# Performance work log

Measured on AMD Instinct MI355X. Metric: run time of the kernel, lower is better.

The kernel has to match this reference:

```python
import jax, jax.numpy as jnp
import numpy as np

NUM_SUBGRAPH = 4096  # static number of segments (subgraph_idx.max() + 1)


def setup_inputs() -> dict:
    key = jax.random.key(0)
    k1, k2, k3, k4 = jax.random.split(key, 4)
    E, K = 4194304, 20
    label = jax.random.randint(k1, (E,), 0, 2).astype(jnp.float32)      # 0/1 edge labels
    log_theta = jax.random.normal(k2, (E, K), dtype=jnp.float32)        # Bernoulli logits per mixture comp
    log_alpha = jax.random.normal(k3, (E, K), dtype=jnp.float32)        # mixture logits per edge
    subgraph_idx = jax.random.randint(k4, (E,), 0, NUM_SUBGRAPH)        # segment id per edge
    return {"label": label, "log_theta": log_theta, "log_alpha": log_alpha,
            "subgraph_idx": subgraph_idx}


def reference(label, log_theta, log_alpha, subgraph_idx):
    E, K = log_theta.shape
    S = NUM_SUBGRAPH
    # BCEWithLogits(reduction='none'), vectorized over all K components:
    # softplus(x) - x*y  ==  -(y*log sigmoid(x) + (1-y)*log(1-sigmoid(x)))
    adj_loss = jax.nn.softplus(log_theta) - log_theta * label[:, None]  # [E, K]
    # segment reductions keyed by subgraph_idx
    const = jax.ops.segment_sum(jnp.ones((E,), log_theta.dtype), subgraph_idx,
                                num_segments=S)                          # [S]
    reduce_adj_loss = jax.ops.segment_sum(adj_loss, subgraph_idx,
                                          num_segments=S)                # [S, K]
    reduce_log_alpha = jax.ops.segment_sum(log_alpha, subgraph_idx,
                                           num_segments=S)               # [S, K]
    reduce_log_alpha = reduce_log_alpha / const[:, None]
    reduce_log_alpha = jax.nn.log_softmax(reduce_log_alpha, axis=-1)
    log_prob = jax.scipy.special.logsumexp(-reduce_adj_loss + reduce_log_alpha, axis=1)  # [S]
    loss = -jnp.sum(log_prob) / jnp.asarray(E, log_theta.dtype)
    return loss
```

## Files before the change

kernel.cpp:

```cpp
#include <hip/hip_runtime.h>
#include <stdint.h>


#define S_SEG 4096
#define K_COMP 20

__device__ __forceinline__ float sp_f(float x) {
    return fmaxf(x, 0.f) + __logf(1.f + __expf(-fabsf(x)));
}

__device__ __forceinline__ void gatomic_add_f(float* p, float v) {
    __hip_atomic_fetch_add(p, v, __ATOMIC_RELAXED, __HIP_MEMORY_SCOPE_AGENT);
}

__global__ __launch_bounds__(256) void pack_count_kernel(
    const int* __restrict__ sidx, const float* __restrict__ label,
    unsigned short* __restrict__ packed, unsigned int* __restrict__ g_cnt,
    int E4, int doPack)
{
    __shared__ unsigned int hist[S_SEG];
    for (int i = threadIdx.x; i < S_SEG; i += 256) hist[i] = 0u;
    __syncthreads();

    const int4*   s4 = (const int4*)sidx;
    const float4* l4 = (const float4*)label;
    int gt = blockIdx.x * 256 + threadIdx.x;
    int stride = gridDim.x * 256;
    for (int i = gt; i < E4; i += stride) {
        int4   sv = s4[i];
        float4 lv = l4[i];
        atomicAdd(&hist[sv.x & 4095], 1u);
        atomicAdd(&hist[sv.y & 4095], 1u);
        atomicAdd(&hist[sv.z & 4095], 1u);
        atomicAdd(&hist[sv.w & 4095], 1u);
        if (doPack) {
            ushort4 pk;
            pk.x = (unsigned short)((sv.x & 4095) | (lv.x != 0.f ? 0x8000 : 0));
            pk.y = (unsigned short)((sv.y & 4095) | (lv.y != 0.f ? 0x8000 : 0));
            pk.z = (unsigned short)((sv.z & 4095) | (lv.z != 0.f ? 0x8000 : 0));
            pk.w = (unsigned short)((sv.w & 4095) | (lv.w != 0.f ? 0x8000 : 0));
            ((ushort4*)packed)[i] = pk;
        }
    }
    __syncthreads();
    for (int i = threadIdx.x; i < S_SEG; i += 256) {
        unsigned int c = hist[i];
        if (c) atomicAdd(&g_cnt[i], c);
    }
}

template<bool PACKED>
__global__ __launch_bounds__(256) void seg_accum_kernel(
    const float* __restrict__ theta, const float* __restrict__ alpha,
    const unsigned short* __restrict__ packed,
    const int* __restrict__ sidx, const float* __restrict__ label,
    float* __restrict__ g_adj, float* __restrict__ g_alp,
    int ntiles)
{
    __shared__ float tab[4 * S_SEG];
    for (int i = threadIdx.x; i < 4 * S_SEG; i += 256) tab[i] = 0.f;
    __syncthreads();

    const int  role  = blockIdx.x;
    const bool isAdj = role < 5;
    const int  c4    = isAdj ? role : role - 5;
    const float4* src4 = (const float4*)(isAdj ? theta : alpha);
    const int nY = gridDim.y;

    for (int t = blockIdx.y; t < ntiles; t += 2 * nY) {
        const int tB = t + nY;
        const bool hasB = (tB < ntiles);

        int eA = t * 256 + threadIdx.x;
        float4 vA = src4[(size_t)eA * 5 + c4];
        int sA; float labA;
        if (PACKED) {
            unsigned short p = packed[eA];
            sA = p & 4095; labA = (p & 0x8000) ? 1.f : 0.f;
        } else {
            sA = sidx[eA] & 4095; labA = label[eA];
        }

        int eB = 0; float4 vB; int sB = 0; float labB = 0.f;
        if (hasB) {
            eB = tB * 256 + threadIdx.x;
            vB = src4[(size_t)eB * 5 + c4];
            if (PACKED) {
                unsigned short p = packed[eB];
                sB = p & 4095; labB = (p & 0x8000) ? 1.f : 0.f;
            } else {
                sB = sidx[eB] & 4095; labB = label[eB];
            }
        }

        if (isAdj) {
            vA.x = sp_f(vA.x) - vA.x * labA;
            vA.y = sp_f(vA.y) - vA.y * labA;
            vA.z = sp_f(vA.z) - vA.z * labA;
            vA.w = sp_f(vA.w) - vA.w * labA;
        }
        atomicAdd(&tab[            sA], vA.x);
        atomicAdd(&tab[1 * S_SEG + sA], vA.y);
        atomicAdd(&tab[2 * S_SEG + sA], vA.z);
        atomicAdd(&tab[3 * S_SEG + sA], vA.w);

        if (hasB) {
            if (isAdj) {
                vB.x = sp_f(vB.x) - vB.x * labB;
                vB.y = sp_f(vB.y) - vB.y * labB;
                vB.z = sp_f(vB.z) - vB.z * labB;
                vB.w = sp_f(vB.w) - vB.w * labB;
            }
            atomicAdd(&tab[            sB], vB.x);
            atomicAdd(&tab[1 * S_SEG + sB], vB.y);
            atomicAdd(&tab[2 * S_SEG + sB], vB.z);
            atomicAdd(&tab[3 * S_SEG + sB], vB.w);
        }
    }
    __syncthreads();

    float* g = isAdj ? g_adj : g_alp;
    const int k0 = c4 * 4;
    for (int j = threadIdx.x; j < 4 * S_SEG; j += 256) {
        int kk = j >> 12;
        int s  = j & 4095;
        gatomic_add_f(&g[s * K_COMP + k0 + kk], tab[j]);
    }
}

__global__ __launch_bounds__(256) void finalize_kernel(
    const float* __restrict__ g_adj, const float* __restrict__ g_alp,
    const unsigned int* __restrict__ g_cnt, float* __restrict__ out, float Ef)
{
    float local = 0.f;
    for (int s = threadIdx.x; s < S_SEG; s += 256) {
        float c = (float)g_cnt[s];
        if (c < 1.f) c = 1.f;
        float inv = 1.f / c;

        float a[K_COMP];
        float am = -1e30f;
        #pragma unroll
        for (int k = 0; k < K_COMP; ++k) {
            a[k] = g_alp[s * K_COMP + k] * inv;
            am = fmaxf(am, a[k]);
        }
        float den = 0.f;
        #pragma unroll
        for (int k = 0; k < K_COMP; ++k) den += __expf(a[k] - am);
        float lse = am + __logf(den);

        float t[K_COMP];
        float tm = -1e30f;
        #pragma unroll
        for (int k = 0; k < K_COMP; ++k) {
            t[k] = (a[k] - lse) - g_adj[s * K_COMP + k];
            tm = fmaxf(tm, t[k]);
        }
        float d2 = 0.f;
        #pragma unroll
        for (int k = 0; k < K_COMP; ++k) d2 += __expf(t[k] - tm);
        local += tm + __logf(d2);
    }

    __shared__ float red[256];
    red[threadIdx.x] = local;
    __syncthreads();
    for (int o = 128; o > 0; o >>= 1) {
        if (threadIdx.x < o) red[threadIdx.x] += red[threadIdx.x + o];
        __syncthreads();
    }
    if (threadIdx.x == 0) out[0] = -red[0] / Ef;
}

extern "C" void kernel_launch(void* const* d_in, const int* in_sizes, int n_in,
                              void* d_out, int out_size, void* d_ws, size_t ws_size,
                              hipStream_t stream)
{
    const float* label = (const float*)d_in[0];
    const float* theta = (const float*)d_in[1];
    const float* alpha = (const float*)d_in[2];
    const int*   sidx  = (const int*)d_in[3];
    const int E = in_sizes[0];

    float* g_adj = (float*)d_ws;
    float* g_alp = g_adj + S_SEG * K_COMP;
    unsigned int* g_cnt = (unsigned int*)(g_alp + S_SEG * K_COMP);
    const size_t tablesBytes = (size_t)S_SEG * K_COMP * 4 * 2 + (size_t)S_SEG * 4;
    unsigned short* packed = (unsigned short*)((char*)d_ws + tablesBytes);
    const int doPack = (ws_size >= tablesBytes + (size_t)E * 2) ? 1 : 0;

    hipMemsetAsync(d_ws, 0, tablesBytes, stream);

    pack_count_kernel<<<256, 256, 0, stream>>>(sidx, label, packed, g_cnt, E / 4, doPack);

    const int ntiles = E / 256;
    dim3 grid(10, 48);
    if (doPack)
        seg_accum_kernel<true><<<grid, 256, 0, stream>>>(theta, alpha, packed, sidx, label,
                                                         g_adj, g_alp, ntiles);
    else
        seg_accum_kernel<false><<<grid, 256, 0, stream>>>(theta, alpha, packed, sidx, label,
                                                          g_adj, g_alp, ntiles);

    finalize_kernel<<<1, 256, 0, stream>>>(g_adj, g_alp, g_cnt, (float*)d_out, (float)E);
}
```

Baseline: 1.664 ms.

## Replace shared-memory atomic segment sums with counting sort and register accumulation

Builds a per-segment histogram, prefix-scans it and scatters edge ids with packed labels into segment-sorted order using global atomics. An accumulate kernel then walks contiguous runs of the sorted list, gathers the full 20-wide theta and alpha rows per edge, keeps running sums in registers and flushes them with global atomics only at segment boundaries. This is meant to remove the heavy LDS atomic traffic of the old per-component tiled kernel. The cost is an extra scatter pass with contended global atomics and random row gathers, and the path needs extra workspace, otherwise it falls back to the old kernel.

Result: slower. 2.007 ms (+20.6%).

```diff
diff --git a/kernel.cpp b/kernel.cpp
--- a/kernel.cpp
+++ b/kernel.cpp
@@ -4,6 +4,7 @@
 
 #define S_SEG 4096
 #define K_COMP 20
+#define TPE 16
 
 __device__ __forceinline__ float sp_f(float x) {
     return fmaxf(x, 0.f) + __logf(1.f + __expf(-fabsf(x)));
@@ -22,31 +23,152 @@
     for (int i = threadIdx.x; i < S_SEG; i += 256) hist[i] = 0u;
     __syncthreads();
 
-    const int4*   s4 = (const int4*)sidx;
-    const float4* l4 = (const float4*)label;
+    const int4* s4 = (const int4*)sidx;
     int gt = blockIdx.x * 256 + threadIdx.x;
     int stride = gridDim.x * 256;
     for (int i = gt; i < E4; i += stride) {
-        int4   sv = s4[i];
-        float4 lv = l4[i];
+        int4 sv = s4[i];
         atomicAdd(&hist[sv.x & 4095], 1u);
         atomicAdd(&hist[sv.y & 4095], 1u);
         atomicAdd(&hist[sv.z & 4095], 1u);
         atomicAdd(&hist[sv.w & 4095], 1u);
-        if (doPack) {
-            ushort4 pk;
-            pk.x = (unsigned short)((sv.x & 4095) | (lv.x != 0.f ? 0x8000 : 0));
-            pk.y = (unsigned short)((sv.y & 4095) | (lv.y != 0.f ? 0x8000 : 0));
-            pk.z = (unsigned short)((sv.z & 4095) | (lv.z != 0.f ? 0x8000 : 0));
-            pk.w = (unsigned short)((sv.w & 4095) | (lv.w != 0.f ? 0x8000 : 0));
-            ((ushort4*)packed)[i] = pk;
-        }
     }
     __syncthreads();
     for (int i = threadIdx.x; i < S_SEG; i += 256) {
         unsigned int c = hist[i];
         if (c) atomicAdd(&g_cnt[i], c);
     }
+    (void)label; (void)packed; (void)doPack;
+}
+
+__global__ __launch_bounds__(1024) void scan_kernel(
+    const unsigned int* __restrict__ g_cnt,
+    unsigned int* __restrict__ g_pref, unsigned int* __restrict__ g_cur)
+{
+    __shared__ unsigned int ts[1024];
+    const int tid = threadIdx.x;
+
+    uint4 c = ((const uint4*)g_cnt)[tid];
+    unsigned s0 = c.x;
+    unsigned s1 = s0 + c.y;
+    unsigned s2 = s1 + c.z;
+    unsigned s3 = s2 + c.w;
+    ts[tid] = s3;
+    __syncthreads();
+
+    for (int off = 1; off < 1024; off <<= 1) {
+        unsigned v = 0;
+        if (tid >= off) v = ts[tid - off];
+        __syncthreads();
+        ts[tid] += v;
+        __syncthreads();
+    }
+
+    unsigned base = ts[tid] - s3;
+    uint4 p;
+    p.x = base;
+    p.y = base + s0;
+    p.z = base + s1;
+    p.w = base + s2;
+    ((uint4*)g_pref)[tid] = p;
+    ((uint4*)g_cur)[tid]  = p;
+    if (tid == 1023) g_pref[S_SEG] = ts[1023];
+}
+
+__global__ __launch_bounds__(256) void scatter_kernel(
+    const int* __restrict__ sidx, const float* __restrict__ label,
+    unsigned int* __restrict__ g_cur, unsigned int* __restrict__ sorted, int E4)
+{
+    const int4*   s4 = (const int4*)sidx;
+    const float4* l4 = (const float4*)label;
+    int i = blockIdx.x * 256 + threadIdx.x;
+    int stride = gridDim.x * 256;
+    for (; i < E4; i += stride) {
+        int4   sv = s4[i];
+        float4 lv = l4[i];
+        unsigned e = (unsigned)i * 4u;
+        unsigned p;
+        p = atomicAdd(&g_cur[sv.x & 4095], 1u); sorted[p] = (e    ) | (lv.x != 0.f ? 0x80000000u : 0u);
+        p = atomicAdd(&g_cur[sv.y & 4095], 1u); sorted[p] = (e + 1) | (lv.y != 0.f ? 0x80000000u : 0u);
+        p = atomicAdd(&g_cur[sv.z & 4095], 1u); sorted[p] = (e + 2) | (lv.z != 0.f ? 0x80000000u : 0u);
+        p = atomicAdd(&g_cur[sv.w & 4095], 1u); sorted[p] = (e + 3) | (lv.w != 0.f ? 0x80000000u : 0u);
+    }
+}
+
+__device__ __forceinline__ void flush_acc(
+    float* __restrict__ g_adj, float* __restrict__ g_alp,
+    int s, const float4 (&aj)[5], const float4 (&al)[5])
+{
+    float* pa = g_adj + (size_t)s * K_COMP;
+    float* pl = g_alp + (size_t)s * K_COMP;
+    #pragma unroll
+    for (int k = 0; k < 5; ++k) {
+        gatomic_add_f(pa + k*4 + 0, aj[k].x);
+        gatomic_add_f(pa + k*4 + 1, aj[k].y);
+        gatomic_add_f(pa + k*4 + 2, aj[k].z);
+        gatomic_add_f(pa + k*4 + 3, aj[k].w);
+        gatomic_add_f(pl + k*4 + 0, al[k].x);
+        gatomic_add_f(pl + k*4 + 1, al[k].y);
+        gatomic_add_f(pl + k*4 + 2, al[k].z);
+        gatomic_add_f(pl + k*4 + 3, al[k].w);
+    }
+}
+
+__global__ __launch_bounds__(256) void accum_kernel(
+    const float* __restrict__ theta, const float* __restrict__ alpha,
+    const unsigned int* __restrict__ sorted, const unsigned int* __restrict__ g_pref,
+    float* __restrict__ g_adj, float* __restrict__ g_alp, int E)
+{
+    __shared__ unsigned int pref[S_SEG + 1];
+    for (int i = threadIdx.x; i < S_SEG + 1; i += 256) pref[i] = g_pref[i];
+    __syncthreads();
+
+    int p0 = (blockIdx.x * 256 + threadIdx.x) * TPE;
+    if (p0 >= E) return;
+    int p1 = p0 + TPE; if (p1 > E) p1 = E;
+
+    int lo = 0, hi = S_SEG;
+    while (hi - lo > 1) {
+        int mid = (lo + hi) >> 1;
+        if (pref[mid] <= (unsigned)p0) lo = mid; else hi = mid;
+    }
+    int s = lo;
+    unsigned nxt = pref[s + 1];
+
+    float4 aj[5], al[5];
+    #pragma unroll
+    for (int k = 0; k < 5; ++k) { aj[k] = make_float4(0,0,0,0); al[k] = make_float4(0,0,0,0); }
+
+    const float4* t4 = (const float4*)theta;
+    const float4* a4 = (const float4*)alpha;
+
+    for (int p = p0; p < p1; ++p) {
+        if ((unsigned)p == nxt) {
+            flush_acc(g_adj, g_alp, s, aj, al);
+            do { ++s; } while (pref[s + 1] <= (unsigned)p);
+            nxt = pref[s + 1];
+            #pragma unroll
+            for (int k = 0; k < 5; ++k) { aj[k] = make_float4(0,0,0,0); al[k] = make_float4(0,0,0,0); }
+        }
+        unsigned pay = sorted[p];
+        unsigned e   = pay & 0x7fffffffu;
+        float    lab = (pay & 0x80000000u) ? 1.f : 0.f;
+        size_t   b   = (size_t)e * 5;
+        #pragma unroll
+        for (int k = 0; k < 5; ++k) {
+            float4 tv = t4[b + k];
+            float4 av = a4[b + k];
+            aj[k].x += sp_f(tv.x) - tv.x * lab;
+            aj[k].y += sp_f(tv.y) - tv.y * lab;
+            aj[k].z += sp_f(tv.z) - tv.z * lab;
+            aj[k].w += sp_f(tv.w) - tv.w * lab;
+            al[k].x += av.x;
+            al[k].y += av.y;
+            al[k].z += av.z;
+            al[k].w += av.w;
+        }
+    }
+    flush_acc(g_adj, g_alp, s, aj, al);
 }
 
 template<bool PACKED>
@@ -67,32 +189,11 @@
     const float4* src4 = (const float4*)(isAdj ? theta : alpha);
     const int nY = gridDim.y;
 
-    for (int t = blockIdx.y; t < ntiles; t += 2 * nY) {
-        const int tB = t + nY;
-        const bool hasB = (tB < ntiles);
-
+    for (int t = blockIdx.y; t < ntiles; t += nY) {
         int eA = t * 256 + threadIdx.x;
         float4 vA = src4[(size_t)eA * 5 + c4];
-        int sA; float labA;
-        if (PACKED) {
-            unsigned short p = packed[eA];
-            sA = p & 4095; labA = (p & 0x8000) ? 1.f : 0.f;
-        } else {
-            sA = sidx[eA] & 4095; labA = label[eA];
-        }
-
-        int eB = 0; float4 vB; int sB = 0; float labB = 0.f;
-        if (hasB) {
-            eB = tB * 256 + threadIdx.x;
-            vB = src4[(size_t)eB * 5 + c4];
-            if (PACKED) {
-                unsigned short p = packed[eB];
-                sB = p & 4095; labB = (p & 0x8000) ? 1.f : 0.f;
-            } else {
-                sB = sidx[eB] & 4095; labB = label[eB];
-            }
-        }
-
+        int sA = sidx[eA] & 4095;
+        float labA = label[eA];
         if (isAdj) {
             vA.x = sp_f(vA.x) - vA.x * labA;
             vA.y = sp_f(vA.y) - vA.y * labA;
@@ -103,19 +204,6 @@
         atomicAdd(&tab[1 * S_SEG + sA], vA.y);
         atomicAdd(&tab[2 * S_SEG + sA], vA.z);
         atomicAdd(&tab[3 * S_SEG + sA], vA.w);
-
-        if (hasB) {
-            if (isAdj) {
-                vB.x = sp_f(vB.x) - vB.x * labB;
-                vB.y = sp_f(vB.y) - vB.y * labB;
-                vB.z = sp_f(vB.z) - vB.z * labB;
-                vB.w = sp_f(vB.w) - vB.w * labB;
-            }
-            atomicAdd(&tab[            sB], vB.x);
-            atomicAdd(&tab[1 * S_SEG + sB], vB.y);
-            atomicAdd(&tab[2 * S_SEG + sB], vB.z);
-            atomicAdd(&tab[3 * S_SEG + sB], vB.w);
-        }
     }
     __syncthreads();
 
@@ -123,9 +211,10 @@
     const int k0 = c4 * 4;
     for (int j = threadIdx.x; j < 4 * S_SEG; j += 256) {
         int kk = j >> 12;
-        int s  = j & 4095;
-        gatomic_add_f(&g[s * K_COMP + k0 + kk], tab[j]);
-    }
+        int ss = j & 4095;
+        gatomic_add_f(&g[ss * K_COMP + k0 + kk], tab[j]);
+    }
+    (void)packed;
 }
 
 __global__ __launch_bounds__(256) void finalize_kernel(
@@ -185,23 +274,28 @@
 
     float* g_adj = (float*)d_ws;
     float* g_alp = g_adj + S_SEG * K_COMP;
-    unsigned int* g_cnt = (unsigned int*)(g_alp + S_SEG * K_COMP);
+    unsigned int* g_cnt  = (unsigned int*)(g_alp + S_SEG * K_COMP);
+    unsigned int* g_cur  = g_cnt + S_SEG;
+    unsigned int* g_pref = g_cur + S_SEG;
+    unsigned int* sorted = g_pref + 4160;
     const size_t tablesBytes = (size_t)S_SEG * K_COMP * 4 * 2 + (size_t)S_SEG * 4;
-    unsigned short* packed = (unsigned short*)((char*)d_ws + tablesBytes);
-    const int doPack = (ws_size >= tablesBytes + (size_t)E * 2) ? 1 : 0;
+    const size_t need = tablesBytes + (size_t)S_SEG * 4 + 4160 * 4 + (size_t)E * 4;
 
     hipMemsetAsync(d_ws, 0, tablesBytes, stream);
 
-    pack_count_kernel<<<256, 256, 0, stream>>>(sidx, label, packed, g_cnt, E / 4, doPack);
-
-    const int ntiles = E / 256;
-    dim3 grid(10, 48);
-    if (doPack)
-        seg_accum_kernel<true><<<grid, 256, 0, stream>>>(theta, alpha, packed, sidx, label,
-                                                         g_adj, g_alp, ntiles);
-    else
-        seg_accum_kernel<false><<<grid, 256, 0, stream>>>(theta, alpha, packed, sidx, label,
-                                                          g_adj, g_alp, ntiles);
+    pack_count_kernel<<<256, 256, 0, stream>>>(sidx, label, nullptr, g_cnt, E / 4, 0);
+
+    if (ws_size >= need && (E % 4) == 0) {
+        scan_kernel<<<1, 1024, 0, stream>>>(g_cnt, g_pref, g_cur);
+        scatter_kernel<<<1024, 256, 0, stream>>>(sidx, label, g_cur, sorted, E / 4);
+        int ablocks = (E / TPE + 255) / 256;
+        accum_kernel<<<ablocks, 256, 0, stream>>>(theta, alpha, sorted, g_pref,
+                                                  g_adj, g_alp, E);
+    } else {
+        seg_accum_kernel<false><<<dim3(10, 96), 256, 0, stream>>>(theta, alpha, nullptr,
+                                                                  sidx, label, g_adj, g_alp,
+                                                                  E / 256);
+    }
 
     finalize_kernel<<<1, 256, 0, stream>>>(g_adj, g_alp, g_cnt, (float*)d_out, (float)E);
 }
```

## Transpose inputs into component planes, then reduce via per-block partials

Applied to the files above, without the earlier changes.

When the workspace is large enough, the change first transposes theta (with the BCE loss fused in) and then alpha into component-major planes. Segment sums are accumulated in shared-memory tables, each block writes its own partial table, and a separate kernel reduces the partials, so global atomics and the memset go away. The intent is coalesced float4 reads per component and no global atomic contention. In exchange it adds a full extra write and re-read of the E×K data for each tensor, about 335MB of plane traffic per tensor, and needs a very large workspace. Otherwise it falls back to the old direct path with a larger grid.

After: 1.661 ms. About the same (-0.2%).

```diff
diff --git a/kernel.cpp b/kernel.cpp
--- a/kernel.cpp
+++ b/kernel.cpp
@@ -4,6 +4,9 @@
 
 #define S_SEG 4096
 #define K_COMP 20
+#define THB 1024
+#define RY 102
+#define RT 512
 
 __device__ __forceinline__ float sp_f(float x) {
     return fmaxf(x, 0.f) + __logf(1.f + __expf(-fabsf(x)));
@@ -13,34 +16,137 @@
     __hip_atomic_fetch_add(p, v, __ATOMIC_RELAXED, __HIP_MEMORY_SCOPE_AGENT);
 }
 
-__global__ __launch_bounds__(256) void pack_count_kernel(
-    const int* __restrict__ sidx, const float* __restrict__ label,
-    unsigned short* __restrict__ packed, unsigned int* __restrict__ g_cnt,
-    int E4, int doPack)
+__global__ __launch_bounds__(256) void t1_kernel(
+    const float* __restrict__ theta, const float* __restrict__ label,
+    const int* __restrict__ sidx,
+    float* __restrict__ adjT, unsigned short* __restrict__ packed,
+    unsigned int* __restrict__ part_hist, int E)
 {
     __shared__ unsigned int hist[S_SEG];
     for (int i = threadIdx.x; i < S_SEG; i += 256) hist[i] = 0u;
     __syncthreads();
 
-    const int4*   s4 = (const int4*)sidx;
-    const float4* l4 = (const float4*)label;
+    const float4* t4 = (const float4*)theta;
+    float4*       o4 = (float4*)adjT;
+
+    int gt = blockIdx.x * 256 + threadIdx.x;
+    int stride = gridDim.x * 256;
+    for (int e = gt; e < E; e += stride) {
+        int s = sidx[e] & 4095;
+        float lab = label[e];
+        atomicAdd(&hist[s], 1u);
+        packed[e] = (unsigned short)s;
+        size_t b = (size_t)e * 5;
+        #pragma unroll
+        for (int c = 0; c < 5; ++c) {
+            float4 v = t4[b + c];
+            v.x = sp_f(v.x) - v.x * lab;
+            v.y = sp_f(v.y) - v.y * lab;
+            v.z = sp_f(v.z) - v.z * lab;
+            v.w = sp_f(v.w) - v.w * lab;
+            o4[(size_t)c * E + e] = v;
+        }
+    }
+    __syncthreads();
+    unsigned int* ph = part_hist + (size_t)blockIdx.x * S_SEG;
+    for (int i = threadIdx.x; i < S_SEG; i += 256) ph[i] = hist[i];
+}
+
+__global__ __launch_bounds__(256) void t2_kernel(
+    const float* __restrict__ alpha, float* __restrict__ alpT, int E)
+{
+    const float4* a4 = (const float4*)alpha;
+    float4*       o4 = (float4*)alpT;
+    int gt = blockIdx.x * 256 + threadIdx.x;
+    int stride = gridDim.x * 256;
+    for (int e = gt; e < E; e += stride) {
+        size_t b = (size_t)e * 5;
+        #pragma unroll
+        for (int c = 0; c < 5; ++c) o4[(size_t)c * E + e] = a4[b + c];
+    }
+}
+
+__global__ __launch_bounds__(RT) void r_kernel(
+    const float* __restrict__ planes, const unsigned short* __restrict__ packed,
+    float* __restrict__ partial, int E, int ntiles)
+{
+    __shared__ float tab[4 * S_SEG];
+    for (int i = threadIdx.x; i < 4 * S_SEG; i += RT) tab[i] = 0.f;
+    __syncthreads();
+
+    const int c4 = blockIdx.x;
+    const float4* src = ((const float4*)planes) + (size_t)c4 * E;
+    const int tid = threadIdx.x;
+
+    for (int t = blockIdx.y; t < ntiles; t += 2 * RY) {
+        const int tB = t + RY;
+        const bool hasB = (tB < ntiles);
+
+        int eA = t * RT + tid;
+        bool okA = (eA < E);
+        float4 vA; int sA = 0;
+        if (okA) { vA = src[eA]; sA = packed[eA]; }
+
+        int eB = hasB ? tB * RT + tid : 0;
+        bool okB = hasB && (eB < E);
+        float4 vB; int sB = 0;
+        if (okB) { vB = src[eB]; sB = packed[eB]; }
+
+        if (okA) {
+            atomicAdd(&tab[             sA], vA.x);
+            atomicAdd(&tab[1 * S_SEG + sA], vA.y);
+            atomicAdd(&tab[2 * S_SEG + sA], vA.z);
+            atomicAdd(&tab[3 * S_SEG + sA], vA.w);
+        }
+        if (okB) {
+            atomicAdd(&tab[             sB], vB.x);
+            atomicAdd(&tab[1 * S_SEG + sB], vB.y);
+            atomicAdd(&tab[2 * S_SEG + sB], vB.z);
+            atomicAdd(&tab[3 * S_SEG + sB], vB.w);
+        }
+    }
+    __syncthreads();
+
+    float* p = partial + ((size_t)c4 * RY + blockIdx.y) * (4 * S_SEG);
+    for (int j = threadIdx.x; j < 4 * S_SEG; j += RT) p[j] = tab[j];
+}
+
+__global__ __launch_bounds__(256) void reduce_kernel(
+    const float* __restrict__ partial, const unsigned int* __restrict__ part_hist,
+    float* __restrict__ g_out, unsigned int* __restrict__ g_cnt, int doCnt)
+{
+    int idx = blockIdx.x * 256 + threadIdx.x;
+    if (idx < 5 * 4 * S_SEG) {
+        int s  = idx & 4095;
+        int kk = (idx >> 12) & 3;
+        int c4 = idx >> 14;
+        float acc = 0.f;
+        const float* p = partial + (size_t)c4 * RY * (4 * S_SEG) + kk * S_SEG + s;
+        for (int y = 0; y < RY; ++y) acc += p[(size_t)y * (4 * S_SEG)];
+        g_out[s * K_COMP + c4 * 4 + kk] = acc;
+    }
+    if (doCnt && idx < S_SEG) {
+        unsigned int c = 0;
+        for (int y = 0; y < THB; ++y) c += part_hist[(size_t)y * S_SEG + idx];
+        g_cnt[idx] = c;
+    }
+}
+
+__global__ __launch_bounds__(256) void pack_count_kernel(
+    const int* __restrict__ sidx, unsigned int* __restrict__ g_cnt, int E4)
+{
+    __shared__ unsigned int hist[S_SEG];
+    for (int i = threadIdx.x; i < S_SEG; i += 256) hist[i] = 0u;
+    __syncthreads();
+    const int4* s4 = (const int4*)sidx;
     int gt = blockIdx.x * 256 + threadIdx.x;
     int stride = gridDim.x * 256;
     for (int i = gt; i < E4; i += stride) {
-        int4   sv = s4[i];
-        float4 lv = l4[i];
+        int4 sv = s4[i];
         atomicAdd(&hist[sv.x & 4095], 1u);
         atomicAdd(&hist[sv.y & 4095], 1u);
         atomicAdd(&hist[sv.z & 4095], 1u);
         atomicAdd(&hist[sv.w & 4095], 1u);
-        if (doPack) {
-            ushort4 pk;
-            pk.x = (unsigned short)((sv.x & 4095) | (lv.x != 0.f ? 0x8000 : 0));
-            pk.y = (unsigned short)((sv.y & 4095) | (lv.y != 0.f ? 0x8000 : 0));
-            pk.z = (unsigned short)((sv.z & 4095) | (lv.z != 0.f ? 0x8000 : 0));
-            pk.w = (unsigned short)((sv.w & 4095) | (lv.w != 0.f ? 0x8000 : 0));
-            ((ushort4*)packed)[i] = pk;
-        }
     }
     __syncthreads();
     for (int i = threadIdx.x; i < S_SEG; i += 256) {
@@ -49,13 +155,10 @@
     }
 }
 
-template<bool PACKED>
 __global__ __launch_bounds__(256) void seg_accum_kernel(
     const float* __restrict__ theta, const float* __restrict__ alpha,
-    const unsigned short* __restrict__ packed,
     const int* __restrict__ sidx, const float* __restrict__ label,
-    float* __restrict__ g_adj, float* __restrict__ g_alp,
-    int ntiles)
+    float* __restrict__ g_adj, float* __restrict__ g_alp, int ntiles)
 {
     __shared__ float tab[4 * S_SEG];
     for (int i = threadIdx.x; i < 4 * S_SEG; i += 256) tab[i] = 0.f;
@@ -67,55 +170,21 @@
     const float4* src4 = (const float4*)(isAdj ? theta : alpha);
     const int nY = gridDim.y;
 
-    for (int t = blockIdx.y; t < ntiles; t += 2 * nY) {
-        const int tB = t + nY;
-        const bool hasB = (tB < ntiles);
-
+    for (int t = blockIdx.y; t < ntiles; t += nY) {
         int eA = t * 256 + threadIdx.x;
         float4 vA = src4[(size_t)eA * 5 + c4];
-        int sA; float labA;
-        if (PACKED) {
-            unsigned short p = packed[eA];
-            sA = p & 4095; labA = (p & 0x8000) ? 1.f : 0.f;
-        } else {
-            sA = sidx[eA] & 4095; labA = label[eA];
-        }
-
-        int eB = 0; float4 vB; int sB = 0; float labB = 0.f;
-        if (hasB) {
-            eB = tB * 256 + threadIdx.x;
-            vB = src4[(size_t)eB * 5 + c4];
-            if (PACKED) {
-                unsigned short p = packed[eB];
-                sB = p & 4095; labB = (p & 0x8000) ? 1.f : 0.f;
-            } else {
-                sB = sidx[eB] & 4095; labB = label[eB];
-            }
-        }
-
+        int sA = sidx[eA] & 4095;
+        float labA = label[eA];
         if (isAdj) {
             vA.x = sp_f(vA.x) - vA.x * labA;
             vA.y = sp_f(vA.y) - vA.y * labA;
             vA.z = sp_f(vA.z) - vA.z * labA;
             vA.w = sp_f(vA.w) - vA.w * labA;
         }
-        atomicAdd(&tab[            sA], vA.x);
+        atomicAdd(&tab[             sA], vA.x);
         atomicAdd(&tab[1 * S_SEG + sA], vA.y);
         atomicAdd(&tab[2 * S_SEG + sA], vA.z);
         atomicAdd(&tab[3 * S_SEG + sA], vA.w);
-
-        if (hasB) {
-            if (isAdj) {
-                vB.x = sp_f(vB.x) - vB.x * labB;
-                vB.y = sp_f(vB.y) - vB.y * labB;
-                vB.z = sp_f(vB.z) - vB.z * labB;
-                vB.w = sp_f(vB.w) - vB.w * labB;
-            }
-            atomicAdd(&tab[            sB], vB.x);
-            atomicAdd(&tab[1 * S_SEG + sB], vB.y);
-            atomicAdd(&tab[2 * S_SEG + sB], vB.z);
-            atomicAdd(&tab[3 * S_SEG + sB], vB.w);
-        }
     }
     __syncthreads();
 
@@ -123,8 +192,8 @@
     const int k0 = c4 * 4;
     for (int j = threadIdx.x; j < 4 * S_SEG; j += 256) {
         int kk = j >> 12;
-        int s  = j & 4095;
-        gatomic_add_f(&g[s * K_COMP + k0 + kk], tab[j]);
+        int ss = j & 4095;
+        gatomic_add_f(&g[ss * K_COMP + k0 + kk], tab[j]);
     }
 }
 
@@ -183,25 +252,43 @@
     const int*   sidx  = (const int*)d_in[3];
     const int E = in_sizes[0];
 
-    float* g_adj = (float*)d_ws;
-    float* g_alp = g_adj + S_SEG * K_COMP;
-    unsigned int* g_cnt = (unsigned int*)(g_alp + S_SEG * K_COMP);
-    const size_t tablesBytes = (size_t)S_SEG * K_COMP * 4 * 2 + (size_t)S_SEG * 4;
-    unsigned short* packed = (unsigned short*)((char*)d_ws + tablesBytes);
-    const int doPack = (ws_size >= tablesBytes + (size_t)E * 2) ? 1 : 0;
-
-    hipMemsetAsync(d_ws, 0, tablesBytes, stream);
-
-    pack_count_kernel<<<256, 256, 0, stream>>>(sidx, label, packed, g_cnt, E / 4, doPack);
-
-    const int ntiles = E / 256;
-    dim3 grid(10, 48);
-    if (doPack)
-        seg_accum_kernel<true><<<grid, 256, 0, stream>>>(theta, alpha, packed, sidx, label,
-                                                         g_adj, g_alp, ntiles);
-    else
-        seg_accum_kernel<false><<<grid, 256, 0, stream>>>(theta, alpha, packed, sidx, label,
-                                                          g_adj, g_alp, ntiles);
-
-    finalize_kernel<<<1, 256, 0, stream>>>(g_adj, g_alp, g_cnt, (float*)d_out, (float)E);
-}
+    const size_t planeElems   = (size_t)E * K_COMP;
+    const size_t partialElems = (size_t)5 * RY * 4 * S_SEG;
+    const size_t phElems      = (size_t)THB * S_SEG;
+
+    float*          planeBuf  = (float*)d_ws;
+    float*          partial   = planeBuf + planeElems;
+    unsigned int*   part_hist = (unsigned int*)(partial + partialElems);
+    unsigned short* packed    = (unsigned short*)(part_hist + phElems);
+    float*          g_adj     = (float*)((char*)packed + (((size_t)E * 2 + 255) & ~(size_t)255));
+    float*          g_alp     = g_adj + S_SEG * K_COMP;
+    unsigned int*   g_cnt     = (unsigned int*)(g_alp + S_SEG * K_COMP);
+
+    const size_t need = (size_t)((char*)(g_cnt + S_SEG) - (char*)d_ws);
+
+    if (ws_size >= need) {
+        const int ntiles = (E + RT - 1) / RT;
+        dim3 rgrid(5, RY);
+
+        t1_kernel<<<THB, 256, 0, stream>>>(theta, label, sidx, planeBuf, packed, part_hist, E);
+        r_kernel<<<rgrid, RT, 0, stream>>>(planeBuf, packed, partial, E, ntiles);
+        reduce_kernel<<<320, 256, 0, stream>>>(partial, part_hist, g_adj, g_cnt, 1);
+
+        t2_kernel<<<2048, 256, 0, stream>>>(alpha, planeBuf, E);
+        r_kernel<<<rgrid, RT, 0, stream>>>(planeBuf, packed, partial, E, ntiles);
+        reduce_kernel<<<320, 256, 0, stream>>>(partial, part_hist, g_alp, g_cnt, 0);
+
+        finalize_kernel<<<1, 256, 0, stream>>>(g_adj, g_alp, g_cnt, (float*)d_out, (float)E);
+    } else {
+        float* f_adj = (float*)d_ws;
+        float* f_alp = f_adj + S_SEG * K_COMP;
+        unsigned int* f_cnt = (unsigned int*)(f_alp + S_SEG * K_COMP);
+        const size_t tablesBytes = (size_t)S_SEG * K_COMP * 4 * 2 + (size_t)S_SEG * 4;
+
+        hipMemsetAsync(d_ws, 0, tablesBytes, stream);
+        pack_count_kernel<<<256, 256, 0, stream>>>(sidx, f_cnt, E / 4);
+        seg_accum_kernel<<<dim3(10, 96), 256, 0, stream>>>(theta, alpha, sidx, label,
+                                                           f_adj, f_alp, E / 256);
+        finalize_kernel<<<1, 256, 0, stream>>>(f_adj, f_alp, f_cnt, (float*)d_out, (float)E);
+    }
+}
```
